# Performance work log

Hardware: AMD Instinct MI355X
Metric: run time of the kernel (lower is better)

## Reference

```python
import jax, jax.numpy as jnp
import numpy as np

H, KV, D, HID = 32, 8, 128, 4096  # heads, kv heads, head_dim, hidden
BLOCK = 64
SEQLENS = [512, 768, 512, 256]  # packed continuous batch, T = 2048
NUM_BLOCKS = 64


def setup_inputs() -> dict:
    key = jax.random.key(0)
    ks = jax.random.split(key, 8)
    T = int(sum(SEQLENS))
    position_ids = jnp.asarray(np.concatenate([np.arange(l) for l in SEQLENS]), jnp.int64 if False else jnp.int32)
    seq_ids = jnp.asarray(np.concatenate([np.full(l, b) for b, l in enumerate(SEQLENS)]), jnp.int32)
    # assign cache blocks sequentially per sequence, pad rows with 0 (never read)
    max_blocks = max((l + BLOCK - 1) // BLOCK for l in SEQLENS)
    bo = np.zeros((len(SEQLENS), max_blocks), np.int32)
    nxt = 0
    for b, l in enumerate(SEQLENS):
        nb = (l + BLOCK - 1) // BLOCK
        bo[b, :nb] = np.arange(nxt, nxt + nb)
        nxt += nb
    block_offsets = jnp.asarray(bo)
    vision_mask = jax.random.uniform(ks[0], (T,)) < 0.3
    s = 0.02
    return {
        'hidden_states': jax.random.normal(ks[1], (1, T, HID), jnp.float32),
        'position_ids': position_ids,
        'seq_ids': seq_ids,
        'vision_mask': vision_mask,
        'block_offsets': block_offsets,
        'k_cache': jnp.zeros((NUM_BLOCKS, BLOCK, KV, D), jnp.float32),
        'v_cache': jnp.zeros((NUM_BLOCKS, BLOCK, KV, D), jnp.float32),
        'w_qkv_vision': jax.random.normal(ks[2], (HID, HID + 2 * KV * D), jnp.float32) * s,
        'w_qkv_language': jax.random.normal(ks[3], (HID, HID + 2 * KV * D), jnp.float32) * s,
        'w_dense_vision': jax.random.normal(ks[4], (HID, HID), jnp.float32) * s,
        'w_dense_language': jax.random.normal(ks[5], (HID, HID), jnp.float32) * s,
        'inv_freq': 1.0 / (10000.0 ** (jnp.arange(0, D, 2, dtype=jnp.float32) / D)),
    }


def _rope(x, pos, inv_freq):
    # x: [T, h, D]; rotate-half convention as in lmdeploy fused_rotary_emb
    freqs = pos[:, None].astype(jnp.float32) * inv_freq[None, :]  # [T, D/2]
    cos = jnp.cos(freqs)[:, None, :]
    sin = jnp.sin(freqs)[:, None, :]
    x0, x1 = jnp.split(x, 2, axis=-1)
    return jnp.concatenate([x0 * cos - x1 * sin, x1 * cos + x0 * sin], axis=-1)


def reference(hidden_states, position_ids, seq_ids, vision_mask, block_offsets,
              k_cache, v_cache, w_qkv_vision, w_qkv_language,
              w_dense_vision, w_dense_language, inv_freq):
    T = hidden_states.shape[1]
    x = hidden_states[0]  # [T, HID]
    # masked vision/language expert QKV routing
    qkv = jnp.where(vision_mask[:, None], x @ w_qkv_vision, x @ w_qkv_language)
    q, k, v = jnp.split(qkv, [HID, HID + KV * D], axis=-1)
    q = q.reshape(T, H, D)
    k = k.reshape(T, KV, D)
    v = v.reshape(T, KV, D)
    # fused rotary embedding on q, k
    q = _rope(q, position_ids, inv_freq)
    k = _rope(k, position_ids, inv_freq)
    # fill paged KV cache (scatter), then read K/V back through the cache
    blk = block_offsets[seq_ids, position_ids // BLOCK]  # [T]
    slot = position_ids % BLOCK
    k_cache = k_cache.at[blk, slot].set(k)
    v_cache = v_cache.at[blk, slot].set(v)
    k_used = k_cache[blk, slot]  # [T, KV, D]
    v_used = v_cache[blk, slot]
    # GQA paged attention over the packed ragged batch (block-diag causal)
    qg = q.reshape(T, KV, H // KV, D)
    scale = 1.0 / jnp.sqrt(jnp.asarray(D, jnp.float32))
    scores = jnp.einsum('qhgd,khd->hgqk', qg, k_used) * scale  # [KV,G,T,T]
    mask = (seq_ids[:, None] == seq_ids[None, :]) & (position_ids[None, :] <= position_ids[:, None])
    scores = jnp.where(mask[None, None], scores, jnp.asarray(-1e9, scores.dtype))
    probs = jax.nn.softmax(scores, axis=-1)
    ctx = jnp.einsum('hgqk,khd->qhgd', probs, v_used).reshape(T, HID)
    # masked expert dense routing
    attn = jnp.where(vision_mask[:, None], ctx @ w_dense_vision, ctx @ w_dense_language)
    return attn[None], k_cache, v_cache
```

## Files before the change

### kernel.cpp

```cpp
#include <hip/hip_runtime.h>
#include <hip/hip_bf16.h>
#include <stdint.h>

#define T_TOK 2048
#define HID   4096
#define NH    32
#define NKV   8
#define HD    128
#define NQKV  6144
#define QSCALE 0.08838834764831845f

typedef __bf16 bf16x8 __attribute__((ext_vector_type(8)));
typedef float  f32x4  __attribute__((ext_vector_type(4)));
typedef unsigned short su8 __attribute__((ext_vector_type(8)));
typedef unsigned short su4 __attribute__((ext_vector_type(4)));

__device__ __forceinline__ unsigned short f2bf(float f) {
  union { float f; unsigned u; } x; x.f = f;
  unsigned r = x.u + 0x7FFFu + ((x.u >> 16) & 1u);
  return (unsigned short)(r >> 16);
}
__device__ __forceinline__ float bf2f(unsigned short u) {
  union { unsigned u; float f; } x; x.u = (unsigned)u << 16; return x.f;
}

__device__ __forceinline__ f32x4 mfma16(su8 a, su8 b, f32x4 c) {
  return __builtin_amdgcn_mfma_f32_16x16x32_bf16(
      __builtin_bit_cast(bf16x8, a), __builtin_bit_cast(bf16x8, b), c, 0, 0, 0);
}

#define GLOAD_LDS16(gp, lp)                                                     \
  __builtin_amdgcn_global_load_lds(                                             \
      (const __attribute__((address_space(1))) void*)(gp),                      \
      (__attribute__((address_space(3))) void*)(lp), 16, 0, 0)

__launch_bounds__(256)
__global__ void route_kernel(const int* __restrict__ vm,
                             int* __restrict__ idx_v, int* __restrict__ idx_l,
                             int* __restrict__ cnts) {
  __shared__ int sv[256], sl[256];
  int tid = threadIdx.x;
  int loc[8]; int lv = 0;
  #pragma unroll
  for (int i = 0; i < 8; i++) { loc[i] = (vm[tid * 8 + i] != 0); lv += loc[i]; }
  int ll = 8 - lv;
  sv[tid] = lv; sl[tid] = ll;
  __syncthreads();
  for (int off = 1; off < 256; off <<= 1) {
    int a = (tid >= off) ? sv[tid - off] : 0;
    int b = (tid >= off) ? sl[tid - off] : 0;
    __syncthreads();
    sv[tid] += a; sl[tid] += b;
    __syncthreads();
  }
  int bv = sv[tid] - lv, bl = sl[tid] - ll;
  #pragma unroll
  for (int i = 0; i < 8; i++) {
    int t = tid * 8 + i;
    if (loc[i]) idx_v[bv++] = t; else idx_l[bl++] = t;
  }
  if (tid == 255) { cnts[0] = sv[255]; cnts[1] = sl[255]; }
}

__launch_bounds__(256)
__global__ void convert_wt2(const float* __restrict__ W0, const float* __restrict__ W1,
                            unsigned short* __restrict__ Wt0, unsigned short* __restrict__ Wt1,
                            int N) {
  const float* W = blockIdx.z ? W1 : W0;
  unsigned short* Wt = blockIdx.z ? Wt1 : Wt0;
  __shared__ float tile[64][65];
  int n0 = blockIdx.x * 64, k0 = blockIdx.y * 64;
  int tid = threadIdx.x;
  int tr = tid >> 4, tc4 = (tid & 15) * 4;
  #pragma unroll
  for (int p = 0; p < 4; p++) {
    int k = p * 16 + tr;
    float4 v = *(const float4*)(W + (size_t)(k0 + k) * N + n0 + tc4);
    tile[tc4 + 0][k] = v.x; tile[tc4 + 1][k] = v.y;
    tile[tc4 + 2][k] = v.z; tile[tc4 + 3][k] = v.w;
  }
  __syncthreads();
  int n = tid >> 2, kc = (tid & 3) * 16;
  unsigned short obuf[16];
  #pragma unroll
  for (int j = 0; j < 16; j++) obuf[j] = f2bf(tile[n][kc + j]);
  su8* dst = (su8*)(Wt + (size_t)(n0 + n) * 4096 + k0 + kc);
  dst[0] = *(su8*)&obuf[0];
  dst[1] = *(su8*)&obuf[8];
}

__launch_bounds__(256)
__global__ void convert_x(const float* __restrict__ x,
                          unsigned short* __restrict__ xb, int n8) {
  int i = blockIdx.x * 256 + threadIdx.x;
  if (i < n8) {
    float4 a = ((const float4*)x)[i * 2], b = ((const float4*)x)[i * 2 + 1];
    su8 u = { f2bf(a.x), f2bf(a.y), f2bf(a.z), f2bf(a.w),
              f2bf(b.x), f2bf(b.y), f2bf(b.z), f2bf(b.w) };
    ((su8*)xb)[i] = u;
  }
}

template <bool OBF16>
__launch_bounds__(256)
__global__ void gemm_bf16(const unsigned short* __restrict__ A,
                          const unsigned short* __restrict__ Wv,
                          const unsigned short* __restrict__ Wl,
                          const int* __restrict__ idx_v, const int* __restrict__ idx_l,
                          const int* __restrict__ cnts,
                          void* __restrict__ out, int N) {
  int e = blockIdx.z;
  const unsigned short* Wt = e ? Wl : Wv;
  const int* gidx = e ? idx_l : idx_v;
  int cnt = cnts[e];
  int m0 = blockIdx.y * 128;
  if (cnt == 0 || m0 >= cnt) return;
  int nx = gridDim.x;
  int bx = blockIdx.x;
  int bxs = (nx % 8 == 0) ? ((bx & 7) * (nx >> 3) + (bx >> 3)) : bx;
  int n0 = bxs * 128;

  __shared__ __align__(16) unsigned short a_lds[2][128 * 64];
  __shared__ __align__(16) unsigned short b_lds[2][128 * 64];

  int tid = threadIdx.x;
  int lane = tid & 63;
  int w = tid >> 6;
  int lg = lane >> 4, lr = lane & 15;
  int wm = w >> 1, wn = w & 1;

  int srow = lane >> 3;
  int scolb = ((lane & 7) ^ srow) << 4;
  const char* a_src[4];
  const char* b_src[4];
  #pragma unroll
  for (int j = 0; j < 4; j++) {
    int c = w * 4 + j;
    int r = c * 8 + srow;
    int gr = gidx[min(m0 + r, cnt - 1)];
    a_src[j] = (const char*)(A + (size_t)gr * 4096) + scolb;
    b_src[j] = (const char*)(Wt + (size_t)(n0 + r) * 4096) + scolb;
  }

  f32x4 acc[4][4];
  #pragma unroll
  for (int fm = 0; fm < 4; fm++)
    #pragma unroll
    for (int fn = 0; fn < 4; fn++)
      acc[fm][fn] = (f32x4){0.f, 0.f, 0.f, 0.f};

  auto STAGE = [&](int buf, int kt) {
    size_t kb = (size_t)kt * 128;
    #pragma unroll
    for (int j = 0; j < 4; j++) {
      int c = w * 4 + j;
      GLOAD_LDS16(a_src[j] + kb, (char*)a_lds[buf] + c * 1024);
      GLOAD_LDS16(b_src[j] + kb, (char*)b_lds[buf] + c * 1024);
    }
  };

  STAGE(0, 0);
  STAGE(1, 1);

  for (int t = 0; t < 64; ++t) {
    if (t < 63) { asm volatile("s_waitcnt vmcnt(8)" ::: "memory"); }
    else        { asm volatile("s_waitcnt vmcnt(0)" ::: "memory"); }
    __builtin_amdgcn_s_barrier();
    asm volatile("" ::: "memory");

    const char* la = (const char*)a_lds[t & 1];
    const char* lb = (const char*)b_lds[t & 1];
    su8 af[2][4], bfr[2][4];
    #pragma unroll
    for (int s = 0; s < 2; s++) {
      int colb = s * 64 + lg * 16;
      #pragma unroll
      for (int fm = 0; fm < 4; fm++) {
        int r = wm * 64 + fm * 16 + lr;
        af[s][fm] = *(const su8*)(la + r * 128 + (colb ^ ((r & 7) << 4)));
      }
      #pragma unroll
      for (int fn = 0; fn < 4; fn++) {
        int r = wn * 64 + fn * 16 + lr;
        bfr[s][fn] = *(const su8*)(lb + r * 128 + (colb ^ ((r & 7) << 4)));
      }
    }
    asm volatile("s_waitcnt lgkmcnt(0)" ::: "memory");
    __builtin_amdgcn_sched_barrier(0);
    __builtin_amdgcn_s_barrier();
    asm volatile("" ::: "memory");

    if (t + 2 < 64) STAGE(t & 1, t + 2);
    __builtin_amdgcn_s_setprio(1);
    #pragma unroll
    for (int s = 0; s < 2; s++)
      #pragma unroll
      for (int fm = 0; fm < 4; fm++)
        #pragma unroll
        for (int fn = 0; fn < 4; fn++)
          acc[fm][fn] = mfma16(af[s][fm], bfr[s][fn], acc[fm][fn]);
    __builtin_amdgcn_s_setprio(0);
  }

  #pragma unroll
  for (int fm = 0; fm < 4; fm++) {
    #pragma unroll
    for (int i = 0; i < 4; i++) {
      int r = wm * 64 + fm * 16 + lg * 4 + i;
      if (m0 + r < cnt) {
        int grow = gidx[m0 + r];
        #pragma unroll
        for (int fn = 0; fn < 4; fn++) {
          size_t off = (size_t)grow * N + n0 + wn * 64 + fn * 16 + lr;
          if (OBF16) ((unsigned short*)out)[off] = f2bf(acc[fm][fn][i]);
          else       ((float*)out)[off] = acc[fm][fn][i];
        }
      }
    }
  }
}

__launch_bounds__(256)
__global__ void gemm_gather(const float* __restrict__ X,
                            const float* __restrict__ Wv, const float* __restrict__ Wl,
                            const int* __restrict__ idx_v, const int* __restrict__ idx_l,
                            const int* __restrict__ cnts,
                            float* __restrict__ out, int N) {
  int e = blockIdx.z;
  const float* W = e ? Wl : Wv;
  const int* gidx = e ? idx_l : idx_v;
  int cnt = cnts[e];
  int m0 = blockIdx.y * 128;
  if (cnt == 0 || m0 >= cnt) return;
  int n0 = blockIdx.x * 64;

  __shared__ __align__(16) unsigned short a_lds[128][72];
  __shared__ __align__(16) unsigned short b_lds[64][72];

  int tid = threadIdx.x;
  int lane = tid & 63;
  int w = tid >> 6;
  int lg = lane >> 4, lr = lane & 15;
  int wm = w >> 1, wn = w & 1;

  int ar = tid >> 1;
  int akc = (tid & 1) * 32;
  const float* Arow = X + (size_t)gidx[min(m0 + ar, cnt - 1)] * HID;
  int bk = (tid >> 4) * 4;
  int bj = (tid & 15) * 4;

  f32x4 acc[4][2];
  #pragma unroll
  for (int fm = 0; fm < 4; fm++)
    #pragma unroll
    for (int fn = 0; fn < 2; fn++)
      acc[fm][fn] = (f32x4){0.f, 0.f, 0.f, 0.f};

  for (int k0 = 0; k0 < HID; k0 += 64) {
    {
      const float4* src = (const float4*)(Arow + k0 + akc);
      float4 f[8];
      #pragma unroll
      for (int i = 0; i < 8; i++) f[i] = src[i];
      #pragma unroll
      for (int i = 0; i < 4; i++) {
        float4 a0 = f[2 * i], a1 = f[2 * i + 1];
        su8 u = { f2bf(a0.x), f2bf(a0.y), f2bf(a0.z), f2bf(a0.w),
                  f2bf(a1.x), f2bf(a1.y), f2bf(a1.z), f2bf(a1.w) };
        *(su8*)&a_lds[ar][akc + i * 8] = u;
      }
    }
    {
      const float* Wp = W + (size_t)(k0 + bk) * N + n0 + bj;
      float4 r0 = *(const float4*)(Wp);
      float4 r1 = *(const float4*)(Wp + N);
      float4 r2 = *(const float4*)(Wp + 2 * (size_t)N);
      float4 r3 = *(const float4*)(Wp + 3 * (size_t)N);
      su4 c0 = { f2bf(r0.x), f2bf(r1.x), f2bf(r2.x), f2bf(r3.x) };
      su4 c1 = { f2bf(r0.y), f2bf(r1.y), f2bf(r2.y), f2bf(r3.y) };
      su4 c2 = { f2bf(r0.z), f2bf(r1.z), f2bf(r2.z), f2bf(r3.z) };
      su4 c3 = { f2bf(r0.w), f2bf(r1.w), f2bf(r2.w), f2bf(r3.w) };
      *(su4*)&b_lds[bj + 0][bk] = c0;
      *(su4*)&b_lds[bj + 1][bk] = c1;
      *(su4*)&b_lds[bj + 2][bk] = c2;
      *(su4*)&b_lds[bj + 3][bk] = c3;
    }
    __syncthreads();
    #pragma unroll
    for (int s = 0; s < 64; s += 32) {
      su8 af[4], bfr[2];
      #pragma unroll
      for (int fm = 0; fm < 4; fm++)
        af[fm] = *(const su8*)&a_lds[wm * 64 + fm * 16 + lr][s + lg * 8];
      #pragma unroll
      for (int fn = 0; fn < 2; fn++)
        bfr[fn] = *(const su8*)&b_lds[wn * 32 + fn * 16 + lr][s + lg * 8];
      #pragma unroll
      for (int fm = 0; fm < 4; fm++)
        #pragma unroll
        for (int fn = 0; fn < 2; fn++)
          acc[fm][fn] = mfma16(af[fm], bfr[fn], acc[fm][fn]);
    }
    __syncthreads();
  }
  #pragma unroll
  for (int fm = 0; fm < 4; fm++) {
    #pragma unroll
    for (int i = 0; i < 4; i++) {
      int r = wm * 64 + fm * 16 + lg * 4 + i;
      if (m0 + r < cnt) {
        int grow = gidx[m0 + r];
        #pragma unroll
        for (int fn = 0; fn < 2; fn++)
          out[(size_t)grow * N + n0 + wn * 32 + fn * 16 + lr] = acc[fm][fn][i];
      }
    }
  }
}

__launch_bounds__(256)
__global__ void rope_scatter_bf(const unsigned short* __restrict__ qkv,
                                const int* __restrict__ pos_ids,
                                const int* __restrict__ seq_ids,
                                const int* __restrict__ block_offsets, int max_blocks,
                                const float* __restrict__ inv_freq,
                                unsigned short* __restrict__ q_ws,
                                unsigned short* __restrict__ k_ws,
                                unsigned short* __restrict__ v_ws,
                                float* __restrict__ kc_out, float* __restrict__ vc_out) {
  int t = blockIdx.x;
  int tid = threadIdx.x;
  __shared__ float cs[64], sn[64];
  int pos = pos_ids[t];
  if (tid < 64) {
    float f = (float)pos * inv_freq[tid];
    float s, c;
    sincosf(f, &s, &c);
    cs[tid] = c; sn[tid] = s;
  }
  __syncthreads();
  const unsigned short* row = qkv + (size_t)t * NQKV;
  #pragma unroll
  for (int it = 0; it < 2; it++) {
    int chunk = it * 256 + tid;
    int hh = chunk >> 4;
    int d0 = (chunk & 15) * 8;
    int lo = (d0 < 64);
    int j0 = lo ? d0 : d0 - 64;
    su8 x  = *(const su8*)(row + hh * 128 + d0);
    su8 xp = *(const su8*)(row + hh * 128 + (lo ? d0 + 64 : d0 - 64));
    su8 o;
    #pragma unroll
    for (int jj = 0; jj < 8; jj++) {
      float c = cs[j0 + jj], s = sn[j0 + jj];
      float xv = bf2f(x[jj]), pv = bf2f(xp[jj]);
      float val = lo ? (xv * c - pv * s) : (xv * c + pv * s);
      o[jj] = f2bf(val * QSCALE);
    }
    *(su8*)(q_ws + ((size_t)hh * T_TOK + t) * HD + d0) = o;
  }
  int seq = seq_ids[t];
  int blk = block_offsets[seq * max_blocks + (pos >> 6)];
  int slot = pos & 63;
  int chunk = tid & 127;
  int kvh = chunk >> 4;
  int d0 = (chunk & 15) * 8;
  if (tid < 128) {
    const unsigned short* kr = row + HID;
    int lo = (d0 < 64);
    int j0 = lo ? d0 : d0 - 64;
    su8 x  = *(const su8*)(kr + kvh * 128 + d0);
    su8 xp = *(const su8*)(kr + kvh * 128 + (lo ? d0 + 64 : d0 - 64));
    su8 o;
    float of[8];
    #pragma unroll
    for (int jj = 0; jj < 8; jj++) {
      float c = cs[j0 + jj], s = sn[j0 + jj];
      float xv = bf2f(x[jj]), pv = bf2f(xp[jj]);
      float val = lo ? (xv * c - pv * s) : (xv * c + pv * s);
      of[jj] = val;
      o[jj] = f2bf(val);
    }
    *(su8*)(k_ws + ((size_t)kvh * T_TOK + t) * HD + d0) = o;
    float* kc = kc_out + (((size_t)blk * 64 + slot) * NKV + kvh) * HD + d0;
    *(float4*)kc       = (float4){of[0], of[1], of[2], of[3]};
    *(float4*)(kc + 4) = (float4){of[4], of[5], of[6], of[7]};
  } else {
    const unsigned short* vr = row + HID + NKV * HD;
    su8 x = *(const su8*)(vr + kvh * 128 + d0);
    *(su8*)(v_ws + ((size_t)kvh * T_TOK + t) * HD + d0) = x;
    float* vc = vc_out + (((size_t)blk * 64 + slot) * NKV + kvh) * HD + d0;
    *(float4*)vc       = (float4){bf2f(x[0]), bf2f(x[1]), bf2f(x[2]), bf2f(x[3])};
    *(float4*)(vc + 4) = (float4){bf2f(x[4]), bf2f(x[5]), bf2f(x[6]), bf2f(x[7])};
  }
}

__launch_bounds__(256)
__global__ void rope_scatter(const float* __restrict__ qkv,
                             const int* __restrict__ pos_ids,
                             const int* __restrict__ seq_ids,
                             const int* __restrict__ block_offsets, int max_blocks,
                             const float* __restrict__ inv_freq,
                             unsigned short* __restrict__ q_ws,
                             unsigned short* __restrict__ k_ws,
                             unsigned short* __restrict__ v_ws,
                             float* __restrict__ kc_out, float* __restrict__ vc_out) {
  int t = blockIdx.x;
  int tid = threadIdx.x;
  __shared__ float cs[64], sn[64];
  int pos = pos_ids[t];
  if (tid < 64) {
    float f = (float)pos * inv_freq[tid];
    float s, c;
    sincosf(f, &s, &c);
    cs[tid] = c; sn[tid] = s;
  }
  __syncthreads();
  const float* row = qkv + (size_t)t * NQKV;
  #pragma unroll 4
  for (int it = 0; it < 16; it++) {
    int idx = it * 256 + tid;
    int hh = idx >> 7, d = idx & 127;
    float val;
    if (d < 64) val = row[hh * 128 + d] * cs[d] - row[hh * 128 + d + 64] * sn[d];
    else { int j = d - 64; val = row[hh * 128 + d] * cs[j] + row[hh * 128 + j] * sn[j]; }
    q_ws[((size_t)hh * T_TOK + t) * HD + d] = f2bf(val * QSCALE);
  }
  int seq = seq_ids[t];
  int blk = block_offsets[seq * max_blocks + (pos >> 6)];
  int slot = pos & 63;
  #pragma unroll
  for (int it = 0; it < 4; it++) {
    int idx = it * 256 + tid;
    int kvh = idx >> 7, d = idx & 127;
    const float* kr = row + HID;
    float val;
    if (d < 64) val = kr[kvh * 128 + d] * cs[d] - kr[kvh * 128 + d + 64] * sn[d];
    else { int j = d - 64; val = kr[kvh * 128 + d] * cs[j] + kr[kvh * 128 + j] * sn[j]; }
    kc_out[(((size_t)blk * 64 + slot) * NKV + kvh) * HD + d] = val;
    k_ws[((size_t)kvh * T_TOK + t) * HD + d] = f2bf(val);
  }
  #pragma unroll
  for (int it = 0; it < 4; it++) {
    int idx = it * 256 + tid;
    int kvh = idx >> 7, d = idx & 127;
    float val = row[HID + NKV * HD + idx];
    vc_out[(((size_t)blk * 64 + slot) * NKV + kvh) * HD + d] = val;
    v_ws[((size_t)kvh * T_TOK + t) * HD + d] = f2bf(val);
  }
}

template <bool BF16OUT>
__launch_bounds__(256)
__global__ void attn_kernel(const unsigned short* __restrict__ q_ws,
                            const unsigned short* __restrict__ k_ws,
                            const unsigned short* __restrict__ v_ws,
                            const int* __restrict__ pos_ids,
                            void* __restrict__ ctx) {
  int qt = blockIdx.x;
  int h = blockIdx.y;
  int kvh = h >> 2;
  int t0 = qt * 64;

  __shared__ __align__(16) unsigned short q_lds[64][136];
  __shared__ __align__(16) unsigned short k_lds[64][136];
  __shared__ __align__(16) unsigned short v_lds[128][72];
  __shared__ __align__(16) unsigned short p_lds[4][16][72];

  int tid = threadIdx.x;
  int lane = tid & 63;
  int w = tid >> 6;
  int lg = lane >> 4, lr = lane & 15;

  int seq_start = t0 - pos_ids[t0];
  int nkb = (t0 - seq_start) / 64 + 1;

  {
    int r = tid >> 2, dc = (tid & 3) * 32;
    const su8* src = (const su8*)(q_ws + ((size_t)h * T_TOK + t0 + r) * HD + dc);
    #pragma unroll
    for (int i = 0; i < 4; i++) *(su8*)&q_lds[r][dc + i * 8] = src[i];
  }
  __syncthreads();
  su8 qf[4];
  #pragma unroll
  for (int s = 0; s < 4; s++)
    qf[s] = *(const su8*)&q_lds[w * 16 + lr][s * 32 + lg * 8];

  f32x4 O[8];
  #pragma unroll
  for (int fd = 0; fd < 8; fd++) O[fd] = (f32x4){0.f, 0.f, 0.f, 0.f};
  float m_i[4] = { -1e30f, -1e30f, -1e30f, -1e30f };
  float l_i[4] = { 0.f, 0.f, 0.f, 0.f };

  for (int kb = 0; kb < nkb; kb++) {
    int kt0 = seq_start + kb * 64;
    __syncthreads();
    {
      int r = tid >> 2, dc = (tid & 3) * 32;
      const su8* src = (const su8*)(k_ws + ((size_t)kvh * T_TOK + kt0 + r) * HD + dc);
      #pragma unroll
      for (int i = 0; i < 4; i++) *(su8*)&k_lds[r][dc + i * 8] = src[i];
    }
    {
      int d0 = (tid & 31) * 4, key0 = (tid >> 5) * 8;
      su4 vv[8];
      #pragma unroll
      for (int r = 0; r < 8; r++)
        vv[r] = *(const su4*)(v_ws + ((size_t)kvh * T_TOK + kt0 + key0 + r) * HD + d0);
      #pragma unroll
      for (int dd = 0; dd < 4; dd++) {
        su8 u = { vv[0][dd], vv[1][dd], vv[2][dd], vv[3][dd],
                  vv[4][dd], vv[5][dd], vv[6][dd], vv[7][dd] };
        *(su8*)&v_lds[d0 + dd][key0] = u;
      }
    }
    __syncthreads();

    f32x4 S[4];
    #pragma unroll
    for (int f = 0; f < 4; f++) S[f] = (f32x4){0.f, 0.f, 0.f, 0.f};
    __builtin_amdgcn_s_setprio(1);
    #pragma unroll
    for (int f = 0; f < 4; f++) {
      #pragma unroll
      for (int s = 0; s < 4; s++) {
        su8 kf = *(const su8*)&k_lds[f * 16 + lr][s * 32 + lg * 8];
        S[f] = mfma16(qf[s], kf, S[f]);
      }
    }
    __builtin_amdgcn_s_setprio(0);
    if (kt0 == t0) {
      #pragma unroll
      for (int f = 0; f < 4; f++)
        #pragma unroll
        for (int i = 0; i < 4; i++)
          if (f * 16 + lr > w * 16 + lg * 4 + i) S[f][i] = -1e30f;
    }
    float mnew[4], alpha[4];
    #pragma unroll
    for (int i = 0; i < 4; i++) {
      float mx = fmaxf(fmaxf(S[0][i], S[1][i]), fmaxf(S[2][i], S[3][i]));
      #pragma unroll
      for (int off = 8; off > 0; off >>= 1) mx = fmaxf(mx, __shfl_xor(mx, off, 16));
      mnew[i] = fmaxf(m_i[i], mx);
      alpha[i] = __expf(m_i[i] - mnew[i]);
      m_i[i] = mnew[i];
    }
    float rs[4] = { 0.f, 0.f, 0.f, 0.f };
    #pragma unroll
    for (int f = 0; f < 4; f++)
      #pragma unroll
      for (int i = 0; i < 4; i++) {
        float p = __expf(S[f][i] - mnew[i]);
        S[f][i] = p;
        rs[i] += p;
      }
    #pragma unroll
    for (int i = 0; i < 4; i++) {
      #pragma unroll
      for (int off = 8; off > 0; off >>= 1) rs[i] += __shfl_xor(rs[i], off, 16);
      l_i[i] = l_i[i] * alpha[i] + rs[i];
    }
    #pragma unroll
    for (int f = 0; f < 4; f++)
      #pragma unroll
      for (int i = 0; i < 4; i++)
        p_lds[w][lg * 4 + i][f * 16 + lr] = f2bf(S[f][i]);
    #pragma unroll
    for (int fd = 0; fd < 8; fd++)
      #pragma unroll
      for (int i = 0; i < 4; i++)
        O[fd][i] *= alpha[i];
    __builtin_amdgcn_s_setprio(1);
    #pragma unroll
    for (int kk = 0; kk < 2; kk++) {
      su8 pf = *(const su8*)&p_lds[w][lr][kk * 32 + lg * 8];
      #pragma unroll
      for (int fd = 0; fd < 8; fd++) {
        su8 vf = *(const su8*)&v_lds[fd * 16 + lr][kk * 32 + lg * 8];
        O[fd] = mfma16(pf, vf, O[fd]);
      }
    }
    __builtin_amdgcn_s_setprio(0);
  }

  #pragma unroll
  for (int i = 0; i < 4; i++) {
    float inv = 1.f / l_i[i];
    int tq = t0 + w * 16 + lg * 4 + i;
    #pragma unroll
    for (int fd = 0; fd < 8; fd++) {
      size_t off = (size_t)tq * HID + h * HD + fd * 16 + lr;
      if (BF16OUT) ((unsigned short*)ctx)[off] = f2bf(O[fd][i] * inv);
      else ((float*)ctx)[off] = O[fd][i] * inv;
    }
  }
}

extern "C" void kernel_launch(void* const* d_in, const int* in_sizes, int n_in,
                              void* d_out, int out_size, void* d_ws, size_t ws_size,
                              hipStream_t stream) {
  const float* hidden = (const float*)d_in[0];
  const int* pos = (const int*)d_in[1];
  const int* seq = (const int*)d_in[2];
  const int* vmask = (const int*)d_in[3];
  const int* bo = (const int*)d_in[4];
  const float* kc_in = (const float*)d_in[5];
  const float* vc_in = (const float*)d_in[6];
  const float* wqv = (const float*)d_in[7];
  const float* wql = (const float*)d_in[8];
  const float* wdv = (const float*)d_in[9];
  const float* wdl = (const float*)d_in[10];
  const float* invf = (const float*)d_in[11];
  int max_blocks = in_sizes[4] / 4;

  float* out_attn = (float*)d_out;
  float* kc_out = out_attn + (size_t)T_TOK * HID;
  float* vc_out = kc_out + (size_t)4194304;

  (void)hipMemcpyAsync(kc_out, kc_in, (size_t)4194304 * 4, hipMemcpyDeviceToDevice, stream);
  (void)hipMemcpyAsync(vc_out, vc_in, (size_t)4194304 * 4, hipMemcpyDeviceToDevice, stream);

  char* ws = (char*)d_ws;
  const size_t WT_BYTES   = 100663296;
  const size_t R0_BYTES   = 67108864;
  const size_t REQ = WT_BYTES + R0_BYTES + 16777216  + 2 * 4194304  + 32768;

  if (ws_size >= REQ) {
    unsigned short* wt0   = (unsigned short*)ws;
    unsigned short* wt_qv = wt0;
    unsigned short* wt_ql = wt0 + (size_t)25165824;
    unsigned short* wt_dv = wt0;
    unsigned short* wt_dl = wt0 + (size_t)16777216;
    unsigned short* qkv_bf = (unsigned short*)(ws + WT_BYTES);
    unsigned short* ctx_bf = qkv_bf;
    unsigned short* x_bf  = (unsigned short*)(ws + WT_BYTES + 25165824 * 2);
    unsigned short* q_ws  = (unsigned short*)(ws + WT_BYTES + R0_BYTES);
    unsigned short* k_ws  = q_ws + (size_t)NH * T_TOK * HD;
    unsigned short* v_ws  = k_ws + (size_t)NKV * T_TOK * HD;
    int* idx_v = (int*)(v_ws + (size_t)NKV * T_TOK * HD);
    int* idx_l = idx_v + T_TOK;
    int* cnts  = idx_l + T_TOK;

    route_kernel<<<1, 256, 0, stream>>>(vmask, idx_v, idx_l, cnts);
    convert_wt2<<<dim3(96, 64, 2), 256, 0, stream>>>(wqv, wql, wt_qv, wt_ql, NQKV);
    convert_x<<<4096, 256, 0, stream>>>(hidden, x_bf, T_TOK * HID / 8);
    gemm_bf16<true><<<dim3(NQKV / 128, 16, 2), 256, 0, stream>>>(
        x_bf, wt_qv, wt_ql, idx_v, idx_l, cnts, (void*)qkv_bf, NQKV);
    rope_scatter_bf<<<T_TOK, 256, 0, stream>>>(
        qkv_bf, pos, seq, bo, max_blocks, invf, q_ws, k_ws, v_ws, kc_out, vc_out);
    convert_wt2<<<dim3(64, 64, 2), 256, 0, stream>>>(wdv, wdl, wt_dv, wt_dl, HID);
    attn_kernel<true><<<dim3(T_TOK / 64, NH), 256, 0, stream>>>(
        q_ws, k_ws, v_ws, pos, (void*)ctx_bf);
    gemm_bf16<false><<<dim3(HID / 128, 16, 2), 256, 0, stream>>>(
        ctx_bf, wt_dv, wt_dl, idx_v, idx_l, cnts, (void*)out_attn, HID);
  } else {
    float* qkv_ws = (float*)ws;
    float* ctx_ws = (float*)ws;
    size_t off = (size_t)T_TOK * NQKV * 4;
    unsigned short* q_ws = (unsigned short*)(ws + off);
    unsigned short* k_ws = q_ws + (size_t)NH * T_TOK * HD;
    unsigned short* v_ws = k_ws + (size_t)NKV * T_TOK * HD;
    int* idx_v = (int*)(v_ws + (size_t)NKV * T_TOK * HD);
    int* idx_l = idx_v + T_TOK;
    int* cnts = idx_l + T_TOK;

    route_kernel<<<1, 256, 0, stream>>>(vmask, idx_v, idx_l, cnts);
    gemm_gather<<<dim3(NQKV / 64, 16, 2), 256, 0, stream>>>(
        hidden, wqv, wql, idx_v, idx_l, cnts, qkv_ws, NQKV);
    rope_scatter<<<T_TOK, 256, 0, stream>>>(
        qkv_ws, pos, seq, bo, max_blocks, invf, q_ws, k_ws, v_ws, kc_out, vc_out);
    attn_kernel<false><<<dim3(T_TOK / 64, NH), 256, 0, stream>>>(
        q_ws, k_ws, v_ws, pos, (void*)ctx_ws);
    gemm_gather<<<dim3(HID / 64, 16, 2), 256, 0, stream>>>(
        ctx_ws, wdv, wdl, idx_v, idx_l, cnts, out_attn, HID);
  }
}
```

Before: 427.1 us.

## Double-buffer MFMA operand fragments in registers to overlap LDS reads with compute

Restructures the bf16 GEMM main loop so the A and B fragments for the next K-tile are read from LDS into a second register set while MFMAs run on the current set. The loop is unrolled by two so the register buffers alternate, with a prologue that loads the first fragments. The per-iteration wait becomes a full vmcnt(0) before staging, placed ahead of the fragment reads. The aim is to hide LDS read latency behind matrix-core work. In exchange it roughly doubles the fragment register footprint, which may reduce occupancy, and it weakens global-load overlap because each iteration now waits for all outstanding loads.

```diff
diff --git a/kernel.cpp b/kernel.cpp
--- a/kernel.cpp
+++ b/kernel.cpp
@@ -159,48 +159,66 @@
     }
   };
 
+  su8 fA[2][2][4], fB[2][2][4];
+
+#define READ_FRAGS(P, BUF) do {                                                  \
+    const char* la_ = (const char*)a_lds[BUF];                                   \
+    const char* lb_ = (const char*)b_lds[BUF];                                   \
+    _Pragma("unroll")                                                            \
+    for (int s_ = 0; s_ < 2; s_++) {                                             \
+      int colb_ = s_ * 64 + lg * 16;                                             \
+      _Pragma("unroll")                                                          \
+      for (int fm_ = 0; fm_ < 4; fm_++) {                                        \
+        int r_ = wm * 64 + fm_ * 16 + lr;                                        \
+        fA[P][s_][fm_] = *(const su8*)(la_ + r_ * 128 + (colb_ ^ ((r_ & 7) << 4))); \
+      }                                                                          \
+      _Pragma("unroll")                                                          \
+      for (int fn_ = 0; fn_ < 4; fn_++) {                                        \
+        int r_ = wn * 64 + fn_ * 16 + lr;                                        \
+        fB[P][s_][fn_] = *(const su8*)(lb_ + r_ * 128 + (colb_ ^ ((r_ & 7) << 4))); \
+      }                                                                          \
+    }                                                                            \
+  } while (0)
+
+#define ITER_BODY(T, PC, PN) do {                                                \
+    asm volatile("s_waitcnt vmcnt(0)" ::: "memory");                             \
+    __builtin_amdgcn_s_barrier();                                                \
+    asm volatile("" ::: "memory");                                               \
+    if ((T) + 2 < 64) STAGE((T) & 1, (T) + 2);                                   \
+    if ((T) + 1 < 64) READ_FRAGS(PN, ((T) + 1) & 1);                             \
+    __builtin_amdgcn_s_setprio(1);                                               \
+    _Pragma("unroll")                                                            \
+    for (int s_ = 0; s_ < 2; s_++)                                               \
+      _Pragma("unroll")                                                          \
+      for (int fm_ = 0; fm_ < 4; fm_++)                                          \
+        _Pragma("unroll")                                                        \
+        for (int fn_ = 0; fn_ < 4; fn_++)                                        \
+          acc[fm_][fn_] = mfma16(fA[PC][s_][fm_], fB[PC][s_][fn_], acc[fm_][fn_]); \
+    __builtin_amdgcn_s_setprio(0);                                               \
+    asm volatile("s_waitcnt lgkmcnt(0)" ::: "memory");                           \
+    __builtin_amdgcn_sched_barrier(0);                                           \
+    __builtin_amdgcn_s_barrier();                                                \
+    asm volatile("" ::: "memory");                                               \
+  } while (0)
+
   STAGE(0, 0);
   STAGE(1, 1);
-
-  for (int t = 0; t < 64; ++t) {
-    if (t < 63) { asm volatile("s_waitcnt vmcnt(8)" ::: "memory"); }
-    else        { asm volatile("s_waitcnt vmcnt(0)" ::: "memory"); }
-    __builtin_amdgcn_s_barrier();
-    asm volatile("" ::: "memory");
-
-    const char* la = (const char*)a_lds[t & 1];
-    const char* lb = (const char*)b_lds[t & 1];
-    su8 af[2][4], bfr[2][4];
-    #pragma unroll
-    for (int s = 0; s < 2; s++) {
-      int colb = s * 64 + lg * 16;
-      #pragma unroll
-      for (int fm = 0; fm < 4; fm++) {
-        int r = wm * 64 + fm * 16 + lr;
-        af[s][fm] = *(const su8*)(la + r * 128 + (colb ^ ((r & 7) << 4)));
-      }
-      #pragma unroll
-      for (int fn = 0; fn < 4; fn++) {
-        int r = wn * 64 + fn * 16 + lr;
-        bfr[s][fn] = *(const su8*)(lb + r * 128 + (colb ^ ((r & 7) << 4)));
-      }
-    }
-    asm volatile("s_waitcnt lgkmcnt(0)" ::: "memory");
-    __builtin_amdgcn_sched_barrier(0);
-    __builtin_amdgcn_s_barrier();
-    asm volatile("" ::: "memory");
-
-    if (t + 2 < 64) STAGE(t & 1, t + 2);
-    __builtin_amdgcn_s_setprio(1);
-    #pragma unroll
-    for (int s = 0; s < 2; s++)
-      #pragma unroll
-      for (int fm = 0; fm < 4; fm++)
-        #pragma unroll
-        for (int fn = 0; fn < 4; fn++)
-          acc[fm][fn] = mfma16(af[s][fm], bfr[s][fn], acc[fm][fn]);
-    __builtin_amdgcn_s_setprio(0);
-  }
+  asm volatile("s_waitcnt vmcnt(8)" ::: "memory");
+  __builtin_amdgcn_s_barrier();
+  asm volatile("" ::: "memory");
+  READ_FRAGS(0, 0);
+  asm volatile("s_waitcnt lgkmcnt(0)" ::: "memory");
+  __builtin_amdgcn_sched_barrier(0);
+  __builtin_amdgcn_s_barrier();
+  asm volatile("" ::: "memory");
+
+  #pragma unroll 1
+  for (int t = 0; t < 64; t += 2) {
+    ITER_BODY(t, 0, 1);
+    ITER_BODY(t + 1, 1, 0);
+  }
+#undef READ_FRAGS
+#undef ITER_BODY
 
   #pragma unroll
   for (int fm = 0; fm < 4; fm++) {
```

After: 652.7 us. 1.53x slower.

## Double-buffer K/V tiles in attention with async global-to-LDS K loads

Applied to the files above, without the earlier changes.

The attention kernel now keeps two LDS buffers for K and V. It prefetches the next key block while computing on the current one, with K loaded straight into LDS through a GLOAD_LDS16 path and V held in registers until the end of the iteration. K is stored in an XOR-swizzled layout to avoid LDS bank conflicts, and Q staging reuses the second V buffer. The goal is to hide global load latency behind the MFMA work. The cost is more LDS and registers, which could lower occupancy, plus manual waitcnt and barrier handling that needs to be correct.

```diff
diff --git a/kernel.cpp b/kernel.cpp
--- a/kernel.cpp
+++ b/kernel.cpp
@@ -462,10 +462,10 @@
   int kvh = h >> 2;
   int t0 = qt * 64;
 
-  __shared__ __align__(16) unsigned short q_lds[64][136];
-  __shared__ __align__(16) unsigned short k_lds[64][136];
-  __shared__ __align__(16) unsigned short v_lds[128][72];
+  __shared__ __align__(16) unsigned short k_lds[2][64 * 128];
+  __shared__ __align__(16) unsigned short v_lds[2][128][72];
   __shared__ __align__(16) unsigned short p_lds[4][16][72];
+  unsigned short* q_lds = &v_lds[1][0][0];
 
   int tid = threadIdx.x;
   int lane = tid & 63;
@@ -475,17 +475,59 @@
   int seq_start = t0 - pos_ids[t0];
   int nkb = (t0 - seq_start) / 64 + 1;
 
+  const char* kbase = (const char*)(k_ws + (size_t)kvh * T_TOK * HD);
+  int krow_l[4], ksrc_off[4];
+  #pragma unroll
+  for (int j = 0; j < 4; j++) {
+    int c = w * 4 + j;
+    int r = c * 4 + (lane >> 4);
+    krow_l[j] = r;
+    ksrc_off[j] = r * 256 + (((lane & 15) ^ (r & 7)) << 4);
+  }
+  auto K_STAGE = [&](int buf, int kt0) {
+    const char* src = kbase + (size_t)kt0 * 256;
+    #pragma unroll
+    for (int j = 0; j < 4; j++) {
+      int c = w * 4 + j;
+      GLOAD_LDS16(src + ksrc_off[j], (char*)k_lds[buf] + c * 1024 + (lane & 63) * 16);
+    }
+  };
+  int vd0 = (tid & 31) * 4, vkey0 = (tid >> 5) * 8;
+  su4 vv[8];
+  auto V_LOAD = [&](int kt0) {
+    #pragma unroll
+    for (int r = 0; r < 8; r++)
+      vv[r] = *(const su4*)(v_ws + ((size_t)kvh * T_TOK + kt0 + vkey0 + r) * HD + vd0);
+  };
+  auto V_WRITE = [&](int buf) {
+    #pragma unroll
+    for (int dd = 0; dd < 4; dd++) {
+      su8 u = { vv[0][dd], vv[1][dd], vv[2][dd], vv[3][dd],
+                vv[4][dd], vv[5][dd], vv[6][dd], vv[7][dd] };
+      *(su8*)&v_lds[buf][vd0 + dd][vkey0] = u;
+    }
+  };
+
   {
     int r = tid >> 2, dc = (tid & 3) * 32;
     const su8* src = (const su8*)(q_ws + ((size_t)h * T_TOK + t0 + r) * HD + dc);
     #pragma unroll
-    for (int i = 0; i < 4; i++) *(su8*)&q_lds[r][dc + i * 8] = src[i];
-  }
+    for (int i = 0; i < 4; i++) *(su8*)&q_lds[r * 136 + dc + i * 8] = src[i];
+  }
+  K_STAGE(0, seq_start);
+  V_LOAD(seq_start);
   __syncthreads();
   su8 qf[4];
   #pragma unroll
   for (int s = 0; s < 4; s++)
-    qf[s] = *(const su8*)&q_lds[w * 16 + lr][s * 32 + lg * 8];
+    qf[s] = *(const su8*)&q_lds[(w * 16 + lr) * 136 + s * 32 + lg * 8];
+  asm volatile("s_waitcnt lgkmcnt(0)" ::: "memory");
+  __builtin_amdgcn_sched_barrier(0);
+  __builtin_amdgcn_s_barrier();
+  asm volatile("s_waitcnt vmcnt(0)" ::: "memory");
+  V_WRITE(0);
+  asm volatile("" ::: "memory");
+  __syncthreads();
 
   f32x4 O[8];
   #pragma unroll
@@ -494,38 +536,24 @@
   float l_i[4] = { 0.f, 0.f, 0.f, 0.f };
 
   for (int kb = 0; kb < nkb; kb++) {
+    int cur = kb & 1, nxt = cur ^ 1;
     int kt0 = seq_start + kb * 64;
-    __syncthreads();
-    {
-      int r = tid >> 2, dc = (tid & 3) * 32;
-      const su8* src = (const su8*)(k_ws + ((size_t)kvh * T_TOK + kt0 + r) * HD + dc);
-      #pragma unroll
-      for (int i = 0; i < 4; i++) *(su8*)&k_lds[r][dc + i * 8] = src[i];
-    }
-    {
-      int d0 = (tid & 31) * 4, key0 = (tid >> 5) * 8;
-      su4 vv[8];
-      #pragma unroll
-      for (int r = 0; r < 8; r++)
-        vv[r] = *(const su4*)(v_ws + ((size_t)kvh * T_TOK + kt0 + key0 + r) * HD + d0);
-      #pragma unroll
-      for (int dd = 0; dd < 4; dd++) {
-        su8 u = { vv[0][dd], vv[1][dd], vv[2][dd], vv[3][dd],
-                  vv[4][dd], vv[5][dd], vv[6][dd], vv[7][dd] };
-        *(su8*)&v_lds[d0 + dd][key0] = u;
-      }
-    }
-    __syncthreads();
-
+    if (kb + 1 < nkb) {
+      K_STAGE(nxt, kt0 + 64);
+      V_LOAD(kt0 + 64);
+    }
+
+    const char* kl = (const char*)k_lds[cur];
     f32x4 S[4];
     #pragma unroll
     for (int f = 0; f < 4; f++) S[f] = (f32x4){0.f, 0.f, 0.f, 0.f};
     __builtin_amdgcn_s_setprio(1);
     #pragma unroll
     for (int f = 0; f < 4; f++) {
+      int r = f * 16 + lr;
       #pragma unroll
       for (int s = 0; s < 4; s++) {
-        su8 kf = *(const su8*)&k_lds[f * 16 + lr][s * 32 + lg * 8];
+        su8 kf = *(const su8*)(kl + r * 256 + ((s * 64 + lg * 16) ^ ((r & 7) << 4)));
         S[f] = mfma16(qf[s], kf, S[f]);
       }
     }
@@ -578,11 +606,18 @@
       su8 pf = *(const su8*)&p_lds[w][lr][kk * 32 + lg * 8];
       #pragma unroll
       for (int fd = 0; fd < 8; fd++) {
-        su8 vf = *(const su8*)&v_lds[fd * 16 + lr][kk * 32 + lg * 8];
+        su8 vf = *(const su8*)&v_lds[cur][fd * 16 + lr][kk * 32 + lg * 8];
         O[fd] = mfma16(pf, vf, O[fd]);
       }
     }
     __builtin_amdgcn_s_setprio(0);
+
+    if (kb + 1 < nkb) {
+      asm volatile("s_waitcnt vmcnt(0)" ::: "memory");
+      V_WRITE(nxt);
+      asm volatile("" ::: "memory");
+    }
+    __syncthreads();
   }
 
   #pragma unroll
@@ -625,7 +660,7 @@
   char* ws = (char*)d_ws;
   const size_t WT_BYTES   = 100663296;
   const size_t R0_BYTES   = 67108864;
-  const size_t REQ = WT_BYTES + R0_BYTES + 16777216  + 2 * 4194304  + 32768;
+  const size_t REQ  = WT_BYTES + R0_BYTES + 16777216  + 2 * 4194304  + 32768;
 
   if (ws_size >= REQ) {
     unsigned short* wt0   = (unsigned short*)ws;
```

Result: no change. 429.2 us (+0.5%).
